# Kernel optimization log

Hardware: AMD Instinct MI355X
Metric: run time of the kernel (lower is better)

The kernel has to match this reference:

```python
import jax, jax.numpy as jnp
import numpy as np

N, F_IN, H, E, G = 100000, 128, 64, 1600000, 256
BN_EPS = 1e-5


def setup_inputs() -> dict:
    key = jax.random.key(0)
    ks = jax.random.split(key, 32)
    rn = lambda k, shp, s=0.1: jax.random.normal(k, shp, jnp.float32) * s
    ru = lambda k, shp: jax.random.uniform(k, shp, jnp.float32)
    inp = {
        'x': jax.random.normal(ks[0], (N, F_IN), jnp.float32),
        'edge_index': jax.random.randint(ks[1], (2, E), 0, N),
        'batch': jnp.sort(jax.random.randint(ks[2], (N,), 0, G)),
        'w0': rn(ks[3], (F_IN, H)), 'b0': rn(ks[4], (H,)),
        'w1': rn(ks[5], (H, H)), 'b1': rn(ks[6], (H,)),
        'w2': rn(ks[7], (H, H)), 'b2': rn(ks[8], (H,)),
        'g0': ru(ks[9], (H,)) + 0.5, 'beta0': rn(ks[10], (H,)),
        'm0': rn(ks[11], (H,)), 'v0': ru(ks[12], (H,)) + 0.5,
        'g1': ru(ks[13], (H,)) + 0.5, 'beta1': rn(ks[14], (H,)),
        'm1': rn(ks[15], (H,)), 'v1': ru(ks[16], (H,)) + 0.5,
        'g2': ru(ks[17], (H,)) + 0.5, 'beta2': rn(ks[18], (H,)),
        'm2': rn(ks[19], (H,)), 'v2': ru(ks[20], (H,)) + 0.5,
        'l1w': rn(ks[21], (H, H // 2)), 'l1b': rn(ks[22], (H // 2,)),
        'l2w': rn(ks[23], (H // 2, 2)), 'l2b': rn(ks[24], (2,)),
    }
    return inp


def reference(x, edge_index, batch, w0, b0, w1, b1, w2, b2,
              g0, beta0, m0, v0, g1, beta1, m1, v1, g2, beta2, m2, v2,
              l1w, l1b, l2w, l2b):
    n = x.shape[0]
    # GCN: add self-loops, symmetric normalization deg^{-1/2} A_hat deg^{-1/2}
    loop = jnp.arange(n)
    src = jnp.concatenate([edge_index[0], loop])
    dst = jnp.concatenate([edge_index[1], loop])
    deg = jax.ops.segment_sum(jnp.ones_like(src, dtype=x.dtype), dst, num_segments=n)
    dinv = jax.lax.rsqrt(jnp.maximum(deg, 1.0))  # deg >= 1 after self-loops
    norm = (dinv[src] * dinv[dst])[:, None]      # [E+N, 1]

    def gcn(h, w, b):
        h = h @ w                                              # [N, H]
        agg = jax.ops.segment_sum(h[src] * norm, dst, num_segments=n)
        return agg + b

    def bn(h, g, be, m, v):  # eval-mode BatchNorm1d (running stats)
        return (h - m) * (g * jax.lax.rsqrt(v + BN_EPS)) + be

    h = jax.nn.relu(bn(gcn(x, w0, b0), g0, beta0, m0, v0))
    h = jax.nn.relu(bn(gcn(h, w1, b1), g1, beta1, m1, v1))
    h = jax.nn.relu(bn(gcn(h, w2, b2), g2, beta2, m2, v2))
    pooled = jax.ops.segment_sum(h, batch, num_segments=G)     # global_add_pool
    h = jax.nn.relu(pooled @ l1w + l1b)
    return h @ l2w + l2b                                        # [G, 2]
```

## Files before the change

### kernel.cpp

```cpp
#include <hip/hip_runtime.h>
#include <hip/hip_bf16.h>

#define BN_EPS 1e-5f

typedef short bf16x8 __attribute__((ext_vector_type(8)));
typedef float f32x4 __attribute__((ext_vector_type(4)));

static __device__ __forceinline__ unsigned short f2bf(float f) {
    unsigned u = __float_as_uint(f);
    unsigned r = (u + 0x7FFF + ((u >> 16) & 1)) >> 16;
    return (unsigned short)r;
}
static __device__ __forceinline__ float bf2f(unsigned short s) {
    return __uint_as_float((unsigned)s << 16);
}
__device__ __forceinline__ int pad4i(int c) { return (c + 3) & ~3; }

#define BIN_SHIFT 9
#define BIN_NODES 512
#define P1_CHUNK 8192
#define P1_THREADS 1024
#define P1_PER_THREAD (P1_CHUNK / P1_THREADS)
#define IMG_CAP 12288
#define P2_THREADS 512

__global__ void scan_block_exclusive(const int* __restrict__ in, int* __restrict__ out, int m) {
    __shared__ int sd[256];
    int t = threadIdx.x;
    int base = t * 4;
    int v0 = (base + 0 < m) ? in[base + 0] : 0;
    int v1 = (base + 1 < m) ? in[base + 1] : 0;
    int v2 = (base + 2 < m) ? in[base + 2] : 0;
    int v3 = (base + 3 < m) ? in[base + 3] : 0;
    int tsum = v0 + v1 + v2 + v3;
    sd[t] = tsum;
    __syncthreads();
    for (int off = 1; off < 256; off <<= 1) {
        int x = (t >= off) ? sd[t - off] : 0;
        __syncthreads();
        sd[t] += x;
        __syncthreads();
    }
    int excl = sd[t] - tsum;
    if (base + 0 < m) out[base + 0] = excl;
    if (base + 1 < m) out[base + 1] = excl + v0;
    if (base + 2 < m) out[base + 2] = excl + v0 + v1;
    if (base + 3 < m) out[base + 3] = excl + v0 + v1 + v2;
    if (t == 255) out[m] = sd[255];
}

__global__ __launch_bounds__(P1_THREADS) void phase1_kernel(
        const int* __restrict__ src, const int* __restrict__ dst,
        int* __restrict__ bincur, int* __restrict__ ebuf, int e, int ecap) {
    __shared__ int hist[256], base[256], cur[256];
    int t = threadIdx.x;
    int c0 = blockIdx.x * P1_CHUNK;
    int iend = c0 + P1_CHUNK; if (iend > e) iend = e;
    if (t < 256) hist[t] = 0;
    __syncthreads();
    int dreg[P1_PER_THREAD];
#pragma unroll
    for (int u = 0; u < P1_PER_THREAD; u++) {
        int i = c0 + t + u * P1_THREADS;
        if (i < iend) {
            int d = dst[i];
            dreg[u] = d;
            atomicAdd(&hist[d >> BIN_SHIFT], 1);
        }
    }
    __syncthreads();
    if (t < 256) {
        if (hist[t] > 0)
            base[t] = t * ecap + atomicAdd(&bincur[t], hist[t]);
        cur[t] = 0;
    }
    __syncthreads();
#pragma unroll
    for (int u = 0; u < P1_PER_THREAD; u++) {
        int i = c0 + t + u * P1_THREADS;
        if (i < iend) {
            int s = src[i], d = dreg[u];
            int b = d >> BIN_SHIFT;
            int r = atomicAdd(&cur[b], 1);
            int p = base[b] + r;
            if (p < (b + 1) * ecap)
                ebuf[p] = s | ((d & (BIN_NODES - 1)) << 17);
        }
    }
}

__global__ __launch_bounds__(1024) void bincount_kernel(
        const int* __restrict__ ebuf, const int* __restrict__ bincur, int ecap,
        float* __restrict__ dinv, int* __restrict__ row_local,
        int* __restrict__ binpad, unsigned short* __restrict__ ha_sent, int n) {
    __shared__ int c512[BIN_NODES];
    __shared__ int sd[256];
    int b = blockIdx.x, t = threadIdx.x;
    if (b == 0 && t < 64) ha_sent[t] = 0;
    if (t < BIN_NODES) c512[t] = 0;
    __syncthreads();
    int cnt_b = bincur[b]; if (cnt_b > ecap) cnt_b = ecap;
    int e0 = b * ecap, e1 = e0 + cnt_b;
    for (int j = e0 + t; j < e1; j += 1024)
        atomicAdd(&c512[ebuf[j] >> 17], 1);
    __syncthreads();
    int n0 = b * BIN_NODES;
    if (t < BIN_NODES) {
        int i = n0 + t;
        if (i < n) dinv[i] = rsqrtf((float)(c512[t] + 1));
    }
    int v0 = 0, v1 = 0, tsum = 0;
    if (t < 256) {
        v0 = pad4i(c512[2 * t]);
        v1 = pad4i(c512[2 * t + 1]);
        tsum = v0 + v1;
        sd[t] = tsum;
    }
    __syncthreads();
    for (int off = 1; off < 256; off <<= 1) {
        int x = 0;
        if (t < 256 && t >= off) x = sd[t - off];
        __syncthreads();
        if (t < 256) sd[t] += x;
        __syncthreads();
    }
    if (t < 256) {
        int excl = sd[t] - tsum;
        row_local[n0 + 2 * t]     = excl;
        row_local[n0 + 2 * t + 1] = excl + v0;
        if (t == 255) binpad[b] = sd[255];
    }
}

__global__ __launch_bounds__(P2_THREADS) void phase2_kernel(
        const int* __restrict__ ebuf, const int* __restrict__ bincur, int ecap,
        const int* __restrict__ row_local, const int* __restrict__ binbase,
        int* __restrict__ row_start, int* __restrict__ csr,
        int* __restrict__ gcursor, int n, int nbins, int sentinel) {
    __shared__ int image[IMG_CAP];
    __shared__ int lcur[BIN_NODES];
    __shared__ int rl[BIN_NODES];
    int b = blockIdx.x, t = threadIdx.x;
    int n0 = b * BIN_NODES;
    int nloc = n - n0; if (nloc > BIN_NODES) nloc = BIN_NODES;
    int rb = binbase[b];
    int rspan = binbase[b + 1] - rb;
    int cnt_b = bincur[b]; if (cnt_b > ecap) cnt_b = ecap;
    int e0 = b * ecap, e1 = e0 + cnt_b;
    if (t < BIN_NODES) {
        rl[t] = row_local[n0 + t];
        lcur[t] = 0;
    }
    __syncthreads();
    for (int k = t; k < nloc; k += P2_THREADS)
        row_start[n0 + k] = rb + rl[k];
    if (b == 0 && t == 0) row_start[n] = binbase[nbins];
    if (rspan <= IMG_CAP) {
        for (int k = t; k < rspan; k += P2_THREADS) image[k] = sentinel;
        __syncthreads();
        for (int j = e0 + t; j < e1; j += P2_THREADS) {
            int en = ebuf[j];
            int s = en & 0x1FFFF;
            int dl = en >> 17;
            int pos = rl[dl] + atomicAdd(&lcur[dl], 1);
            image[pos] = s;
        }
        __syncthreads();
        for (int k = t; k < rspan; k += P2_THREADS) csr[rb + k] = image[k];
    } else {
        for (int k = t; k < nloc; k += P2_THREADS) gcursor[n0 + k] = 0;
        __syncthreads();
        for (int j = e0 + t; j < e1; j += P2_THREADS) {
            int en = ebuf[j];
            int s = en & 0x1FFFF;
            int dl = en >> 17;
            int pos = rb + rl[dl] + atomicAdd(&gcursor[n0 + dl], 1);
            csr[pos] = s;
        }
        __syncthreads();
        for (int k = t; k < nloc; k += P2_THREADS) {
            int node = n0 + k;
            int start = rb + rl[k] + gcursor[node];
            int end = (k < BIN_NODES - 1) ? rb + rl[k + 1] : binbase[b + 1];
            for (int pos = start; pos < end; pos++) csr[pos] = sentinel;
        }
    }
}

template<int K, bool BF16IN>
__global__ __launch_bounds__(256) void lin_mfma(const void* __restrict__ in_,
                                                const float* __restrict__ w,
                                                const float* __restrict__ dinv,
                                                unsigned short* __restrict__ outbf, int n) {
    constexpr int XS = K + 8;
    __shared__ unsigned short xs[64 * XS];
    __shared__ unsigned short wt[64 * XS];
    int t = threadIdx.x;
    int row0 = blockIdx.x * 64;
    int nrows = n - row0; if (nrows > 64) nrows = 64;

    {
        const float4* w4 = (const float4*)w;
        for (int idx = t; idx < K * 16; idx += 256) {
            int k = idx >> 4, c4 = (idx & 15) * 4;
            float4 v = w4[idx];
            wt[(c4 + 0) * XS + k] = f2bf(v.x);
            wt[(c4 + 1) * XS + k] = f2bf(v.y);
            wt[(c4 + 2) * XS + k] = f2bf(v.z);
            wt[(c4 + 3) * XS + k] = f2bf(v.w);
        }
    }
    if constexpr (BF16IN) {
        const uint4* in4 = (const uint4*)((const unsigned short*)in_ + (size_t)row0 * K);
        int total8 = nrows * (K / 8);
        for (int idx = t; idx < total8; idx += 256) {
            int r = idx / (K / 8), kk = idx - r * (K / 8);
            uint4 v = in4[idx];
            *(uint4*)&xs[r * XS + kk * 8] = v;
        }
    } else {
        const float4* in4 = (const float4*)((const float*)in_ + (size_t)row0 * K);
        int total4 = nrows * (K / 4);
        for (int idx = t; idx < total4; idx += 256) {
            int r = idx / (K / 4), kk = idx - r * (K / 4);
            float4 v = in4[idx];
            ushort4 s4;
            s4.x = f2bf(v.x); s4.y = f2bf(v.y); s4.z = f2bf(v.z); s4.w = f2bf(v.w);
            *(ushort4*)&xs[r * XS + kk * 4] = s4;
        }
    }
    __syncthreads();

    int lane = t & 63;
    int wid = t >> 6;
    int quad = lane >> 4;
    int l15 = lane & 15;

    f32x4 acc[4];
#pragma unroll
    for (int cg_ = 0; cg_ < 4; cg_++) acc[cg_] = (f32x4){0.f, 0.f, 0.f, 0.f};

    const unsigned short* xrow = &xs[(wid * 16 + l15) * XS + quad * 8];
#pragma unroll
    for (int kc = 0; kc < K / 32; kc++) {
        bf16x8 bfrag = *(const bf16x8*)(xrow + kc * 32);
#pragma unroll
        for (int cg_ = 0; cg_ < 4; cg_++) {
            bf16x8 afrag = *(const bf16x8*)&wt[(cg_ * 16 + l15) * XS + kc * 32 + quad * 8];
            acc[cg_] = __builtin_amdgcn_mfma_f32_16x16x32_bf16(afrag, bfrag, acc[cg_], 0, 0, 0);
        }
    }

    int grow = row0 + wid * 16 + l15;
    if (grow < n) {
        float dv = dinv[grow];
#pragma unroll
        for (int cg_ = 0; cg_ < 4; cg_++) {
            ushort4 st;
            st.x = f2bf(acc[cg_][0] * dv);
            st.y = f2bf(acc[cg_][1] * dv);
            st.z = f2bf(acc[cg_][2] * dv);
            st.w = f2bf(acc[cg_][3] * dv);
            *(ushort4*)&outbf[(size_t)grow * 64 + cg_ * 16 + quad * 4] = st;
        }
    }
}

__global__ __launch_bounds__(256) void agg_kernel(
        const unsigned short* __restrict__ hs, const int* __restrict__ row_start,
        const int* __restrict__ csr, const float* __restrict__ dinv,
        const float* __restrict__ bias, const float* __restrict__ gam,
        const float* __restrict__ bet, const float* __restrict__ mu,
        const float* __restrict__ var,
        unsigned short* __restrict__ out, int n) {
    int iw = blockIdx.x * 4 + (threadIdx.x >> 6);
    unsigned lane = threadIdx.x & 63;
    if (iw >= n) return;
    int i = __builtin_amdgcn_readfirstlane(iw);
    float acc = bf2f(hs[((unsigned)i << 6) + lane]);
    int rs = __builtin_amdgcn_readfirstlane(row_start[i]);
    int re = __builtin_amdgcn_readfirstlane(row_start[i + 1]);
    int j = rs;
    for (; j + 16 <= re; j += 16) {
        int s0 = __builtin_amdgcn_readfirstlane(csr[j + 0]);
        int s1 = __builtin_amdgcn_readfirstlane(csr[j + 1]);
        int s2 = __builtin_amdgcn_readfirstlane(csr[j + 2]);
        int s3 = __builtin_amdgcn_readfirstlane(csr[j + 3]);
        int s4 = __builtin_amdgcn_readfirstlane(csr[j + 4]);
        int s5 = __builtin_amdgcn_readfirstlane(csr[j + 5]);
        int s6 = __builtin_amdgcn_readfirstlane(csr[j + 6]);
        int s7 = __builtin_amdgcn_readfirstlane(csr[j + 7]);
        int s8 = __builtin_amdgcn_readfirstlane(csr[j + 8]);
        int s9 = __builtin_amdgcn_readfirstlane(csr[j + 9]);
        int sA = __builtin_amdgcn_readfirstlane(csr[j + 10]);
        int sB = __builtin_amdgcn_readfirstlane(csr[j + 11]);
        int sC = __builtin_amdgcn_readfirstlane(csr[j + 12]);
        int sD = __builtin_amdgcn_readfirstlane(csr[j + 13]);
        int sE = __builtin_amdgcn_readfirstlane(csr[j + 14]);
        int sF = __builtin_amdgcn_readfirstlane(csr[j + 15]);
        float h0 = bf2f(hs[((unsigned)s0 << 6) + lane]);
        float h1 = bf2f(hs[((unsigned)s1 << 6) + lane]);
        float h2 = bf2f(hs[((unsigned)s2 << 6) + lane]);
        float h3 = bf2f(hs[((unsigned)s3 << 6) + lane]);
        float h4 = bf2f(hs[((unsigned)s4 << 6) + lane]);
        float h5 = bf2f(hs[((unsigned)s5 << 6) + lane]);
        float h6 = bf2f(hs[((unsigned)s6 << 6) + lane]);
        float h7 = bf2f(hs[((unsigned)s7 << 6) + lane]);
        float h8 = bf2f(hs[((unsigned)s8 << 6) + lane]);
        float h9 = bf2f(hs[((unsigned)s9 << 6) + lane]);
        float hA = bf2f(hs[((unsigned)sA << 6) + lane]);
        float hB = bf2f(hs[((unsigned)sB << 6) + lane]);
        float hC = bf2f(hs[((unsigned)sC << 6) + lane]);
        float hD = bf2f(hs[((unsigned)sD << 6) + lane]);
        float hE = bf2f(hs[((unsigned)sE << 6) + lane]);
        float hF = bf2f(hs[((unsigned)sF << 6) + lane]);
        acc += (((h0 + h1) + (h2 + h3)) + ((h4 + h5) + (h6 + h7)))
             + (((h8 + h9) + (hA + hB)) + ((hC + hD) + (hE + hF)));
    }
    for (; j < re; j += 4) {
        int s0 = __builtin_amdgcn_readfirstlane(csr[j + 0]);
        int s1 = __builtin_amdgcn_readfirstlane(csr[j + 1]);
        int s2 = __builtin_amdgcn_readfirstlane(csr[j + 2]);
        int s3 = __builtin_amdgcn_readfirstlane(csr[j + 3]);
        float h0 = bf2f(hs[((unsigned)s0 << 6) + lane]);
        float h1 = bf2f(hs[((unsigned)s1 << 6) + lane]);
        float h2 = bf2f(hs[((unsigned)s2 << 6) + lane]);
        float h3 = bf2f(hs[((unsigned)s3 << 6) + lane]);
        acc += (h0 + h1) + (h2 + h3);
    }
    float agg = acc * dinv[i];
    float scale = gam[lane] * rsqrtf(var[lane] + BN_EPS);
    float r = (agg + bias[lane] - mu[lane]) * scale + bet[lane];
    out[((unsigned)i << 6) + lane] = f2bf(r > 0.f ? r : 0.f);
}

#define POOL_CHUNK 64
__global__ __launch_bounds__(256) void pool_kernel(const unsigned short* __restrict__ h,
                                                   const int* __restrict__ batch,
                                                   float* __restrict__ pooled, int n) {
    int wid = blockIdx.x * 4 + (threadIdx.x >> 6);
    int lane = threadIdx.x & 63;
    int start = wid * POOL_CHUNK;
    if (start >= n) return;
    int end = start + POOL_CHUNK; if (end > n) end = n;
    int cur = batch[start];
    float acc = 0.f;
    for (int i = start; i < end; i++) {
        int b = batch[i];
        if (b != cur) {
            atomicAdd(&pooled[(size_t)cur * 64 + lane], acc);
            acc = 0.f; cur = b;
        }
        acc += bf2f(h[(size_t)i * 64 + lane]);
    }
    atomicAdd(&pooled[(size_t)cur * 64 + lane], acc);
}

__global__ void mlp_kernel(const float* __restrict__ pooled,
                           const float* __restrict__ l1w, const float* __restrict__ l1b,
                           const float* __restrict__ l2w, const float* __restrict__ l2b,
                           float* __restrict__ out) {
    int g = blockIdx.x;
    int lane = threadIdx.x;
    __shared__ float p[64];
    __shared__ float h1[32];
    p[lane] = pooled[(size_t)g * 64 + lane];
    __syncthreads();
    if (lane < 32) {
        float a = l1b[lane];
#pragma unroll 8
        for (int k = 0; k < 64; k++) a += p[k] * l1w[k * 32 + lane];
        h1[lane] = a > 0.f ? a : 0.f;
    }
    __syncthreads();
    if (lane < 2) {
        float a = l2b[lane];
#pragma unroll 8
        for (int j = 0; j < 32; j++) a += h1[j] * l2w[j * 2 + lane];
        out[g * 2 + lane] = a;
    }
}

extern "C" void kernel_launch(void* const* d_in, const int* in_sizes, int n_in,
                              void* d_out, int out_size, void* d_ws, size_t ws_size,
                              hipStream_t stream) {
    const float* x     = (const float*)d_in[0];
    const int*   ei    = (const int*)d_in[1];
    const int*   batch = (const int*)d_in[2];
    const float* w0 = (const float*)d_in[3];
    const float* b0 = (const float*)d_in[4];
    const float* w1 = (const float*)d_in[5];
    const float* b1 = (const float*)d_in[6];
    const float* w2 = (const float*)d_in[7];
    const float* b2 = (const float*)d_in[8];
    const float* g0 = (const float*)d_in[9];
    const float* be0 = (const float*)d_in[10];
    const float* m0 = (const float*)d_in[11];
    const float* v0 = (const float*)d_in[12];
    const float* g1 = (const float*)d_in[13];
    const float* be1 = (const float*)d_in[14];
    const float* m1 = (const float*)d_in[15];
    const float* v1 = (const float*)d_in[16];
    const float* g2 = (const float*)d_in[17];
    const float* be2 = (const float*)d_in[18];
    const float* m2 = (const float*)d_in[19];
    const float* v2 = (const float*)d_in[20];
    const float* l1w = (const float*)d_in[21];
    const float* l1b = (const float*)d_in[22];
    const float* l2w = (const float*)d_in[23];
    const float* l2b = (const float*)d_in[24];
    float* out = (float*)d_out;

    const int N = in_sizes[2];
    const int E = in_sizes[1] / 2;
    const int G = out_size / 2;
    const int NBINS = (N + BIN_NODES - 1) / BIN_NODES;
    int ECAP = ((2 * (E / NBINS)) + 1023) & ~1023;
    if (ECAP < 2048) ECAP = 2048;

    const int* src = ei;
    const int* dst = ei + E;

    char* p = (char*)d_ws;
    auto alloc = [&](size_t bytes) -> void* {
        void* r = (void*)p;
        p += (bytes + 255) & ~(size_t)255;
        return r;
    };
    const size_t CSR_CAP = (size_t)E + 4 * (size_t)N + 64;
    float* dinvp    = (float*)alloc((size_t)N * 4);
    int*   row_start= (int*)alloc((size_t)(N + 1) * 4);
    int*   row_local= (int*)alloc((size_t)NBINS * BIN_NODES * 4);
    int*   binpad   = (int*)alloc((size_t)NBINS * 4);
    int*   binbase  = (int*)alloc((size_t)(NBINS + 1) * 4);
    int*   gcursor  = (int*)alloc((size_t)N * 4);
    int*   bincur   = (int*)alloc((size_t)NBINS * 4);
    float* pooled   = (float*)alloc((size_t)G * 64 * 4);
    char*  zero_end = p;
    int*   ebuf     = (int*)alloc((size_t)NBINS * ECAP * 4);
    int*   csr      = (int*)alloc(CSR_CAP * 4);
    unsigned short* h_a = (unsigned short*)alloc((size_t)(N + 1) * 64 * 2);
    unsigned short* h_b = (unsigned short*)alloc((size_t)N * 64 * 2);
    (void)ws_size;

    hipMemsetAsync(bincur, 0, (size_t)(zero_end - (char*)bincur), stream);
    const int nchunks = (E + P1_CHUNK - 1) / P1_CHUNK;
    phase1_kernel<<<nchunks, P1_THREADS, 0, stream>>>(src, dst, bincur, ebuf, E, ECAP);
    bincount_kernel<<<NBINS, 1024, 0, stream>>>(ebuf, bincur, ECAP, dinvp,
                                                row_local, binpad,
                                                h_a + (size_t)N * 64, N);
    scan_block_exclusive<<<1, 256, 0, stream>>>(binpad, binbase, NBINS);
    phase2_kernel<<<NBINS, P2_THREADS, 0, stream>>>(ebuf, bincur, ECAP, row_local,
                                                    binbase, row_start, csr,
                                                    gcursor, N, NBINS, N);

    const int nblk = (N + 3) / 4;
    const int lblk = (N + 63) / 64;
    lin_mfma<128, false><<<lblk, 256, 0, stream>>>(x, w0, dinvp, h_a, N);
    agg_kernel<<<nblk, 256, 0, stream>>>(h_a, row_start, csr, dinvp,
                                         b0, g0, be0, m0, v0, h_b, N);
    lin_mfma<64, true><<<lblk, 256, 0, stream>>>(h_b, w1, dinvp, h_a, N);
    agg_kernel<<<nblk, 256, 0, stream>>>(h_a, row_start, csr, dinvp,
                                         b1, g1, be1, m1, v1, h_b, N);
    lin_mfma<64, true><<<lblk, 256, 0, stream>>>(h_b, w2, dinvp, h_a, N);
    agg_kernel<<<nblk, 256, 0, stream>>>(h_a, row_start, csr, dinvp,
                                         b2, g2, be2, m2, v2, h_b, N);
    const int pwaves = (N + POOL_CHUNK - 1) / POOL_CHUNK;
    pool_kernel<<<(pwaves + 3) / 4, 256, 0, stream>>>(h_b, batch, pooled, N);
    mlp_kernel<<<G, 64, 0, stream>>>(pooled, l1w, l1b, l2w, l2b, out);
}
```

Before: 349.0 us.

## Fuse pooling into last aggregation, vectorize gather, drop bin scan kernel

Bin bases are now assigned with a global atomic counter inside the bincount kernel, which writes row_start and row_len directly. This removes the separate single-block scan kernel and the row_start rewrite in phase2. The aggregation kernel now has each quarter-wave gather a different neighbor with 8-byte loads and combines the partial sums with cross-lane shuffles. The final layer also accumulates the global add pool with atomics, replacing the separate pool kernel. The per-node pool atomics can contend on the same graph rows, and the atomic bin ordering makes the CSR layout nondeterministic.

```diff
diff --git a/kernel.cpp b/kernel.cpp
--- a/kernel.cpp
+++ b/kernel.cpp
@@ -23,31 +23,6 @@
 #define P1_PER_THREAD (P1_CHUNK / P1_THREADS)
 #define IMG_CAP 12288
 #define P2_THREADS 512
-
-__global__ void scan_block_exclusive(const int* __restrict__ in, int* __restrict__ out, int m) {
-    __shared__ int sd[256];
-    int t = threadIdx.x;
-    int base = t * 4;
-    int v0 = (base + 0 < m) ? in[base + 0] : 0;
-    int v1 = (base + 1 < m) ? in[base + 1] : 0;
-    int v2 = (base + 2 < m) ? in[base + 2] : 0;
-    int v3 = (base + 3 < m) ? in[base + 3] : 0;
-    int tsum = v0 + v1 + v2 + v3;
-    sd[t] = tsum;
-    __syncthreads();
-    for (int off = 1; off < 256; off <<= 1) {
-        int x = (t >= off) ? sd[t - off] : 0;
-        __syncthreads();
-        sd[t] += x;
-        __syncthreads();
-    }
-    int excl = sd[t] - tsum;
-    if (base + 0 < m) out[base + 0] = excl;
-    if (base + 1 < m) out[base + 1] = excl + v0;
-    if (base + 2 < m) out[base + 2] = excl + v0 + v1;
-    if (base + 3 < m) out[base + 3] = excl + v0 + v1 + v2;
-    if (t == 255) out[m] = sd[255];
-}
 
 __global__ __launch_bounds__(P1_THREADS) void phase1_kernel(
         const int* __restrict__ src, const int* __restrict__ dst,
@@ -91,10 +66,13 @@
 
 __global__ __launch_bounds__(1024) void bincount_kernel(
         const int* __restrict__ ebuf, const int* __restrict__ bincur, int ecap,
-        float* __restrict__ dinv, int* __restrict__ row_local,
-        int* __restrict__ binpad, unsigned short* __restrict__ ha_sent, int n) {
+        float* __restrict__ dinv, int* __restrict__ row_start,
+        int* __restrict__ row_len, int* __restrict__ binbase,
+        int* __restrict__ binpad, int* __restrict__ gtotal,
+        unsigned short* __restrict__ ha_sent, int n) {
     __shared__ int c512[BIN_NODES];
     __shared__ int sd[256];
+    __shared__ int rbs;
     int b = blockIdx.x, t = threadIdx.x;
     if (b == 0 && t < 64) ha_sent[t] = 0;
     if (t < BIN_NODES) c512[t] = 0;
@@ -124,19 +102,26 @@
         if (t < 256) sd[t] += x;
         __syncthreads();
     }
+    if (t == 0) {
+        int tot = sd[255];
+        int rb = atomicAdd(gtotal, tot);
+        rbs = rb; binbase[b] = rb; binpad[b] = tot;
+    }
+    __syncthreads();
     if (t < 256) {
+        int rb = rbs;
         int excl = sd[t] - tsum;
-        row_local[n0 + 2 * t]     = excl;
-        row_local[n0 + 2 * t + 1] = excl + v0;
-        if (t == 255) binpad[b] = sd[255];
+        int i0 = n0 + 2 * t, i1 = i0 + 1;
+        if (i0 < n) { row_start[i0] = rb + excl;      row_len[i0] = v0; }
+        if (i1 < n) { row_start[i1] = rb + excl + v0; row_len[i1] = v1; }
     }
 }
 
 __global__ __launch_bounds__(P2_THREADS) void phase2_kernel(
         const int* __restrict__ ebuf, const int* __restrict__ bincur, int ecap,
-        const int* __restrict__ row_local, const int* __restrict__ binbase,
-        int* __restrict__ row_start, int* __restrict__ csr,
-        int* __restrict__ gcursor, int n, int nbins, int sentinel) {
+        const int* __restrict__ row_start, const int* __restrict__ row_len,
+        const int* __restrict__ binbase, const int* __restrict__ binpad,
+        int* __restrict__ csr, int* __restrict__ gcursor, int n, int sentinel) {
     __shared__ int image[IMG_CAP];
     __shared__ int lcur[BIN_NODES];
     __shared__ int rl[BIN_NODES];
@@ -144,17 +129,14 @@
     int n0 = b * BIN_NODES;
     int nloc = n - n0; if (nloc > BIN_NODES) nloc = BIN_NODES;
     int rb = binbase[b];
-    int rspan = binbase[b + 1] - rb;
+    int rspan = binpad[b];
     int cnt_b = bincur[b]; if (cnt_b > ecap) cnt_b = ecap;
     int e0 = b * ecap, e1 = e0 + cnt_b;
     if (t < BIN_NODES) {
-        rl[t] = row_local[n0 + t];
+        rl[t] = (t < nloc) ? row_start[n0 + t] - rb : 0;
         lcur[t] = 0;
     }
     __syncthreads();
-    for (int k = t; k < nloc; k += P2_THREADS)
-        row_start[n0 + k] = rb + rl[k];
-    if (b == 0 && t == 0) row_start[n] = binbase[nbins];
     if (rspan <= IMG_CAP) {
         for (int k = t; k < rspan; k += P2_THREADS) image[k] = sentinel;
         __syncthreads();
@@ -180,9 +162,9 @@
         __syncthreads();
         for (int k = t; k < nloc; k += P2_THREADS) {
             int node = n0 + k;
-            int start = rb + rl[k] + gcursor[node];
-            int end = (k < BIN_NODES - 1) ? rb + rl[k + 1] : binbase[b + 1];
-            for (int pos = start; pos < end; pos++) csr[pos] = sentinel;
+            int st = rb + rl[k] + gcursor[node];
+            int en2 = rb + rl[k] + row_len[node];
+            for (int pos = st; pos < en2; pos++) csr[pos] = sentinel;
         }
     }
 }
@@ -266,94 +248,88 @@
     }
 }
 
+template<bool POOL>
 __global__ __launch_bounds__(256) void agg_kernel(
         const unsigned short* __restrict__ hs, const int* __restrict__ row_start,
-        const int* __restrict__ csr, const float* __restrict__ dinv,
+        const int* __restrict__ row_len, const int* __restrict__ csr,
+        const float* __restrict__ dinv,
         const float* __restrict__ bias, const float* __restrict__ gam,
         const float* __restrict__ bet, const float* __restrict__ mu,
         const float* __restrict__ var,
-        unsigned short* __restrict__ out, int n) {
+        unsigned short* __restrict__ out,
+        const int* __restrict__ batch, float* __restrict__ pooled, int n) {
     int iw = blockIdx.x * 4 + (threadIdx.x >> 6);
-    unsigned lane = threadIdx.x & 63;
+    int lane = threadIdx.x & 63;
     if (iw >= n) return;
     int i = __builtin_amdgcn_readfirstlane(iw);
-    float acc = bf2f(hs[((unsigned)i << 6) + lane]);
+    int q = lane >> 4;
+    int m = lane & 15;
+    const unsigned short* hb = hs + (size_t)m * 4;
+    float a0 = 0.f, a1 = 0.f, a2 = 0.f, a3 = 0.f;
+    if (q == 0) {
+        uint2 v = *(const uint2*)(hb + ((size_t)(unsigned)i << 6));
+        a0 += __uint_as_float(v.x << 16);
+        a1 += __uint_as_float(v.x & 0xFFFF0000u);
+        a2 += __uint_as_float(v.y << 16);
+        a3 += __uint_as_float(v.y & 0xFFFF0000u);
+    }
     int rs = __builtin_amdgcn_readfirstlane(row_start[i]);
-    int re = __builtin_amdgcn_readfirstlane(row_start[i + 1]);
+    int re = rs + __builtin_amdgcn_readfirstlane(row_len[i]);
     int j = rs;
     for (; j + 16 <= re; j += 16) {
-        int s0 = __builtin_amdgcn_readfirstlane(csr[j + 0]);
-        int s1 = __builtin_amdgcn_readfirstlane(csr[j + 1]);
-        int s2 = __builtin_amdgcn_readfirstlane(csr[j + 2]);
-        int s3 = __builtin_amdgcn_readfirstlane(csr[j + 3]);
-        int s4 = __builtin_amdgcn_readfirstlane(csr[j + 4]);
-        int s5 = __builtin_amdgcn_readfirstlane(csr[j + 5]);
-        int s6 = __builtin_amdgcn_readfirstlane(csr[j + 6]);
-        int s7 = __builtin_amdgcn_readfirstlane(csr[j + 7]);
-        int s8 = __builtin_amdgcn_readfirstlane(csr[j + 8]);
-        int s9 = __builtin_amdgcn_readfirstlane(csr[j + 9]);
-        int sA = __builtin_amdgcn_readfirstlane(csr[j + 10]);
-        int sB = __builtin_amdgcn_readfirstlane(csr[j + 11]);
-        int sC = __builtin_amdgcn_readfirstlane(csr[j + 12]);
-        int sD = __builtin_amdgcn_readfirstlane(csr[j + 13]);
-        int sE = __builtin_amdgcn_readfirstlane(csr[j + 14]);
-        int sF = __builtin_amdgcn_readfirstlane(csr[j + 15]);
-        float h0 = bf2f(hs[((unsigned)s0 << 6) + lane]);
-        float h1 = bf2f(hs[((unsigned)s1 << 6) + lane]);
-        float h2 = bf2f(hs[((unsigned)s2 << 6) + lane]);
-        float h3 = bf2f(hs[((unsigned)s3 << 6) + lane]);
-        float h4 = bf2f(hs[((unsigned)s4 << 6) + lane]);
-        float h5 = bf2f(hs[((unsigned)s5 << 6) + lane]);
-        float h6 = bf2f(hs[((unsigned)s6 << 6) + lane]);
-        float h7 = bf2f(hs[((unsigned)s7 << 6) + lane]);
-        float h8 = bf2f(hs[((unsigned)s8 << 6) + lane]);
-        float h9 = bf2f(hs[((unsigned)s9 << 6) + lane]);
-        float hA = bf2f(hs[((unsigned)sA << 6) + lane]);
-        float hB = bf2f(hs[((unsigned)sB << 6) + lane]);
-        float hC = bf2f(hs[((unsigned)sC << 6) + lane]);
-        float hD = bf2f(hs[((unsigned)sD << 6) + lane]);
-        float hE = bf2f(hs[((unsigned)sE << 6) + lane]);
-        float hF = bf2f(hs[((unsigned)sF << 6) + lane]);
-        acc += (((h0 + h1) + (h2 + h3)) + ((h4 + h5) + (h6 + h7)))
-             + (((h8 + h9) + (hA + hB)) + ((hC + hD) + (hE + hF)));
+        int s0 = csr[j + q];
+        int s1 = csr[j + 4 + q];
+        int s2 = csr[j + 8 + q];
+        int s3 = csr[j + 12 + q];
+        uint2 v0 = *(const uint2*)(hb + ((size_t)(unsigned)s0 << 6));
+        uint2 v1 = *(const uint2*)(hb + ((size_t)(unsigned)s1 << 6));
+        uint2 v2 = *(const uint2*)(hb + ((size_t)(unsigned)s2 << 6));
+        uint2 v3 = *(const uint2*)(hb + ((size_t)(unsigned)s3 << 6));
+        a0 += __uint_as_float(v0.x << 16);          a1 += __uint_as_float(v0.x & 0xFFFF0000u);
+        a2 += __uint_as_float(v0.y << 16);          a3 += __uint_as_float(v0.y & 0xFFFF0000u);
+        a0 += __uint_as_float(v1.x << 16);          a1 += __uint_as_float(v1.x & 0xFFFF0000u);
+        a2 += __uint_as_float(v1.y << 16);          a3 += __uint_as_float(v1.y & 0xFFFF0000u);
+        a0 += __uint_as_float(v2.x << 16);          a1 += __uint_as_float(v2.x & 0xFFFF0000u);
+        a2 += __uint_as_float(v2.y << 16);          a3 += __uint_as_float(v2.y & 0xFFFF0000u);
+        a0 += __uint_as_float(v3.x << 16);          a1 += __uint_as_float(v3.x & 0xFFFF0000u);
+        a2 += __uint_as_float(v3.y << 16);          a3 += __uint_as_float(v3.y & 0xFFFF0000u);
     }
     for (; j < re; j += 4) {
-        int s0 = __builtin_amdgcn_readfirstlane(csr[j + 0]);
-        int s1 = __builtin_amdgcn_readfirstlane(csr[j + 1]);
-        int s2 = __builtin_amdgcn_readfirstlane(csr[j + 2]);
-        int s3 = __builtin_amdgcn_readfirstlane(csr[j + 3]);
-        float h0 = bf2f(hs[((unsigned)s0 << 6) + lane]);
-        float h1 = bf2f(hs[((unsigned)s1 << 6) + lane]);
-        float h2 = bf2f(hs[((unsigned)s2 << 6) + lane]);
-        float h3 = bf2f(hs[((unsigned)s3 << 6) + lane]);
-        acc += (h0 + h1) + (h2 + h3);
-    }
-    float agg = acc * dinv[i];
-    float scale = gam[lane] * rsqrtf(var[lane] + BN_EPS);
-    float r = (agg + bias[lane] - mu[lane]) * scale + bet[lane];
-    out[((unsigned)i << 6) + lane] = f2bf(r > 0.f ? r : 0.f);
-}
-
-#define POOL_CHUNK 64
-__global__ __launch_bounds__(256) void pool_kernel(const unsigned short* __restrict__ h,
-                                                   const int* __restrict__ batch,
-                                                   float* __restrict__ pooled, int n) {
-    int wid = blockIdx.x * 4 + (threadIdx.x >> 6);
-    int lane = threadIdx.x & 63;
-    int start = wid * POOL_CHUNK;
-    if (start >= n) return;
-    int end = start + POOL_CHUNK; if (end > n) end = n;
-    int cur = batch[start];
-    float acc = 0.f;
-    for (int i = start; i < end; i++) {
-        int b = batch[i];
-        if (b != cur) {
-            atomicAdd(&pooled[(size_t)cur * 64 + lane], acc);
-            acc = 0.f; cur = b;
-        }
-        acc += bf2f(h[(size_t)i * 64 + lane]);
-    }
-    atomicAdd(&pooled[(size_t)cur * 64 + lane], acc);
+        int s0 = csr[j + q];
+        uint2 v0 = *(const uint2*)(hb + ((size_t)(unsigned)s0 << 6));
+        a0 += __uint_as_float(v0.x << 16);          a1 += __uint_as_float(v0.x & 0xFFFF0000u);
+        a2 += __uint_as_float(v0.y << 16);          a3 += __uint_as_float(v0.y & 0xFFFF0000u);
+    }
+    a0 += __shfl_xor(a0, 16); a1 += __shfl_xor(a1, 16);
+    a2 += __shfl_xor(a2, 16); a3 += __shfl_xor(a3, 16);
+    a0 += __shfl_xor(a0, 32); a1 += __shfl_xor(a1, 32);
+    a2 += __shfl_xor(a2, 32); a3 += __shfl_xor(a3, 32);
+    float dv = dinv[i];
+    if (q == 0) {
+        float4 bs4 = *(const float4*)&bias[4 * m];
+        float4 gm4 = *(const float4*)&gam[4 * m];
+        float4 bt4 = *(const float4*)&bet[4 * m];
+        float4 mu4 = *(const float4*)&mu[4 * m];
+        float4 vr4 = *(const float4*)&var[4 * m];
+        float r0 = (a0 * dv + bs4.x - mu4.x) * (gm4.x * rsqrtf(vr4.x + BN_EPS)) + bt4.x;
+        float r1 = (a1 * dv + bs4.y - mu4.y) * (gm4.y * rsqrtf(vr4.y + BN_EPS)) + bt4.y;
+        float r2 = (a2 * dv + bs4.z - mu4.z) * (gm4.z * rsqrtf(vr4.z + BN_EPS)) + bt4.z;
+        float r3 = (a3 * dv + bs4.w - mu4.w) * (gm4.w * rsqrtf(vr4.w + BN_EPS)) + bt4.w;
+        ushort4 st;
+        st.x = f2bf(r0 > 0.f ? r0 : 0.f);
+        st.y = f2bf(r1 > 0.f ? r1 : 0.f);
+        st.z = f2bf(r2 > 0.f ? r2 : 0.f);
+        st.w = f2bf(r3 > 0.f ? r3 : 0.f);
+        *(ushort4*)&out[((size_t)(unsigned)i << 6) + 4 * m] = st;
+        if (POOL) {
+            int g = __builtin_amdgcn_readfirstlane(batch[i]);
+            float* pp = &pooled[(size_t)g * 64 + 4 * m];
+            atomicAdd(pp + 0, bf2f(st.x));
+            atomicAdd(pp + 1, bf2f(st.y));
+            atomicAdd(pp + 2, bf2f(st.z));
+            atomicAdd(pp + 3, bf2f(st.w));
+        }
+    }
 }
 
 __global__ void mlp_kernel(const float* __restrict__ pooled,
@@ -429,12 +405,13 @@
     };
     const size_t CSR_CAP = (size_t)E + 4 * (size_t)N + 64;
     float* dinvp    = (float*)alloc((size_t)N * 4);
-    int*   row_start= (int*)alloc((size_t)(N + 1) * 4);
-    int*   row_local= (int*)alloc((size_t)NBINS * BIN_NODES * 4);
+    int*   row_start= (int*)alloc((size_t)N * 4);
+    int*   row_len  = (int*)alloc((size_t)N * 4);
+    int*   gcursor  = (int*)alloc((size_t)N * 4);
+    int*   binbase  = (int*)alloc((size_t)NBINS * 4);
     int*   binpad   = (int*)alloc((size_t)NBINS * 4);
-    int*   binbase  = (int*)alloc((size_t)(NBINS + 1) * 4);
-    int*   gcursor  = (int*)alloc((size_t)N * 4);
     int*   bincur   = (int*)alloc((size_t)NBINS * 4);
+    int*   gtotal   = (int*)alloc(4);
     float* pooled   = (float*)alloc((size_t)G * 64 * 4);
     char*  zero_end = p;
     int*   ebuf     = (int*)alloc((size_t)NBINS * ECAP * 4);
@@ -447,25 +424,26 @@
     const int nchunks = (E + P1_CHUNK - 1) / P1_CHUNK;
     phase1_kernel<<<nchunks, P1_THREADS, 0, stream>>>(src, dst, bincur, ebuf, E, ECAP);
     bincount_kernel<<<NBINS, 1024, 0, stream>>>(ebuf, bincur, ECAP, dinvp,
-                                                row_local, binpad,
+                                                row_start, row_len, binbase,
+                                                binpad, gtotal,
                                                 h_a + (size_t)N * 64, N);
-    scan_block_exclusive<<<1, 256, 0, stream>>>(binpad, binbase, NBINS);
-    phase2_kernel<<<NBINS, P2_THREADS, 0, stream>>>(ebuf, bincur, ECAP, row_local,
-                                                    binbase, row_start, csr,
-                                                    gcursor, N, NBINS, N);
+    phase2_kernel<<<NBINS, P2_THREADS, 0, stream>>>(ebuf, bincur, ECAP, row_start,
+                                                    row_len, binbase, binpad,
+                                                    csr, gcursor, N, N);
 
     const int nblk = (N + 3) / 4;
     const int lblk = (N + 63) / 64;
     lin_mfma<128, false><<<lblk, 256, 0, stream>>>(x, w0, dinvp, h_a, N);
-    agg_kernel<<<nblk, 256, 0, stream>>>(h_a, row_start, csr, dinvp,
-                                         b0, g0, be0, m0, v0, h_b, N);
+    agg_kernel<false><<<nblk, 256, 0, stream>>>(h_a, row_start, row_len, csr, dinvp,
+                                                b0, g0, be0, m0, v0, h_b,
+                                                batch, pooled, N);
     lin_mfma<64, true><<<lblk, 256, 0, stream>>>(h_b, w1, dinvp, h_a, N);
-    agg_kernel<<<nblk, 256, 0, stream>>>(h_a, row_start, csr, dinvp,
-                                         b1, g1, be1, m1, v1, h_b, N);
+    agg_kernel<false><<<nblk, 256, 0, stream>>>(h_a, row_start, row_len, csr, dinvp,
+                                                b1, g1, be1, m1, v1, h_b,
+                                                batch, pooled, N);
     lin_mfma<64, true><<<lblk, 256, 0, stream>>>(h_b, w2, dinvp, h_a, N);
-    agg_kernel<<<nblk, 256, 0, stream>>>(h_a, row_start, csr, dinvp,
-                                         b2, g2, be2, m2, v2, h_b, N);
-    const int pwaves = (N + POOL_CHUNK - 1) / POOL_CHUNK;
-    pool_kernel<<<(pwaves + 3) / 4, 256, 0, stream>>>(h_b, batch, pooled, N);
+    agg_kernel<true><<<nblk, 256, 0, stream>>>(h_a, row_start, row_len, csr, dinvp,
+                                               b2, g2, be2, m2, v2, h_b,
+                                               batch, pooled, N);
     mlp_kernel<<<G, 64, 0, stream>>>(pooled, l1w, l1b, l2w, l2b, out);
 }
```

Result: slower. 522.6 us (+49.7%).
